# Optimization experiments

Hardware: AMD Instinct MI355X
Metric: run time of the kernel (lower is better)

## Reference

```python
import jax, jax.numpy as jnp
import numpy as np

N = 100_000      # nodes
E = 500_000      # bonds
DN = 128         # dim_node_embedding
DB = 64          # dim_bond_embedding
NTOK = 4         # num_bond_token
DIN = 2 * DN + 2 * DB  # 384
LEAKY = 0.001
LN_EPS = 1e-5
DIST_MAX = 20.0
STEP = 0.5


def _lrelu(v):
    return jnp.where(v >= 0, v, LEAKY * v)


def _layernorm(v, w, b):
    m = v.mean(-1, keepdims=True)
    var = ((v - m) ** 2).mean(-1, keepdims=True)
    return (v - m) / jnp.sqrt(var + LN_EPS) * w + b


def setup_inputs() -> dict:
    key = jax.random.key(0)
    ks = jax.random.split(key, 20)
    x = jax.random.normal(ks[0], (N, 3), dtype=jnp.float32) * 3.0
    pos = jax.random.normal(ks[1], (N, 3), dtype=jnp.float32)
    node_embedding = jax.random.normal(ks[2], (N, DN), dtype=jnp.float32)
    i0 = jax.random.randint(ks[3], (E,), 0, N)
    off = jax.random.randint(ks[4], (E,), 1, N)  # nonzero -> no self-bonds
    bond_index = jnp.stack([i0, (i0 + off) % N], axis=1).astype(jnp.int32)
    bond_types = jax.random.randint(ks[5], (E,), 0, NTOK).astype(jnp.int32)
    s = 0.02
    params = dict(
        bond_emb=jax.random.normal(ks[6], (NTOK, DB), dtype=jnp.float32),
        W0=jax.random.normal(ks[7], (DIN, DN), dtype=jnp.float32) * s,
        b0=jnp.zeros((DN,), jnp.float32),
        W1=jax.random.normal(ks[8], (DN, DN), dtype=jnp.float32) * s,
        b1=jnp.zeros((DN,), jnp.float32),
        ln1_w=jnp.ones((DN,), jnp.float32),
        ln1_b=jnp.zeros((DN,), jnp.float32),
        W2=jax.random.normal(ks[9], (DN, DN), dtype=jnp.float32) * s,
        b2=jnp.zeros((DN,), jnp.float32),
        ln2_w=jnp.ones((DN,), jnp.float32),
        ln2_b=jnp.zeros((DN,), jnp.float32),
        Wo=jax.random.normal(ks[10], (DN, 2), dtype=jnp.float32) * s,
        bo=jnp.zeros((2,), jnp.float32),
    )
    return dict(x=x, pos=pos, node_embedding=node_embedding,
                bond_index=bond_index, bond_types=bond_types, **params)


def reference(x, pos, node_embedding, bond_index, bond_types,
              bond_emb, W0, b0, W1, b1, ln1_w, ln1_b,
              W2, b2, ln2_w, ln2_b, Wo, bo):
    i = bond_index[:, 0]
    j = bond_index[:, 1]

    # ---- BondLength geometry ----
    diff = x[i] - x[j]                                   # [E,3]
    dist = jnp.linalg.norm(diff, axis=-1, keepdims=True)  # [E,1]
    u = diff / dist                                       # [E,3] unit j->i? (i-j)/d
    direction = jnp.stack([u, -u], axis=-1)               # [E,3,2]

    # ---- Smearing (gaussian RBF + overflow bin, normalized) ----
    offset = jnp.linspace(0.0, DIST_MAX, DB - 1, dtype=jnp.float32)  # [63]
    delta = DIST_MAX / (DB - 2)
    coeff = -0.5 / (delta * delta)
    rbf = jnp.exp(coeff * (dist - offset) ** 2)            # [E,63]
    ovf = (dist >= DIST_MAX).astype(x.dtype)               # [E,1]
    smear = jnp.concatenate([rbf, ovf], axis=-1)           # [E,64]
    smear = smear / smear.sum(axis=-1, keepdims=True)

    # ---- Edge MLP (LeakyMLP, num_layer=2, dim_end=2) ----
    feat = jnp.concatenate(
        [node_embedding[i], node_embedding[j], bond_emb[bond_types], smear],
        axis=-1)                                           # [E,384]
    h = _lrelu(feat @ W0 + b0)
    h = _lrelu(_layernorm(h @ W1 + b1, ln1_w, ln1_b))
    h = _lrelu(_layernorm(h @ W2 + b2, ln2_w, ln2_b))
    force = h @ Wo + bo                                    # [E,2]

    # ---- position update (scatter-add) ----
    update = force[:, None, :] * direction                 # [E,3,2]
    pos = pos.at[i].add(STEP * update[..., 0])
    pos = pos.at[j].add(STEP * update[..., 1])
    return pos
```

## Files before the change

kernel.cpp:

```cpp
#include <hip/hip_runtime.h>
#include <stdint.h>

#define N_EDGES 500000
#define N_NODES 100000
#define PREP_NG 2
#define TBINS 1280

typedef __attribute__((ext_vector_type(8))) short short8;
typedef __attribute__((ext_vector_type(4))) float floatx4;

__device__ __forceinline__ uint16_t f2bf(float f) {
  union { float f; uint32_t u; } cv; cv.f = f;
  uint32_t u = cv.u;
  return (uint16_t)((u + 0x7FFFu + ((u >> 16) & 1u)) >> 16);
}
__device__ __forceinline__ uint32_t pk2bf(float lo, float hi) {
  return __builtin_amdgcn_perm(__float_as_uint(hi), __float_as_uint(lo), 0x07060302u);
}
__device__ __forceinline__ uint16_t bftrunc(float f) {
  return (uint16_t)(__float_as_uint(f) >> 16);
}
__device__ __forceinline__ float bf2f_lo(uint32_t u) { return __uint_as_float(u << 16); }
__device__ __forceinline__ float bf2f_hi(uint32_t u) { return __uint_as_float(u & 0xFFFF0000u); }
__device__ __forceinline__ float lrelu(float v) { return fmaxf(v, 0.001f * v); }

__device__ __forceinline__ void gload_lds16(const uint16_t* g, uint16_t* l) {
  __builtin_amdgcn_global_load_lds(
      (const __attribute__((address_space(1))) void*)g,
      (__attribute__((address_space(3))) void*)l, 16, 0, 0);
}

__global__ void prep0_kernel(const float* __restrict__ W0, const float* __restrict__ b0,
                             const float* __restrict__ W1, const float* __restrict__ W2,
                             const float* __restrict__ bemb,
                             uint16_t* __restrict__ w0ab, uint16_t* __restrict__ w1f,
                             uint16_t* __restrict__ w2f, float* __restrict__ be0f,
                             const float* __restrict__ pos, float* __restrict__ out, int npos) {
  int id = blockIdx.x * 256 + threadIdx.x;
  if (id < 32768) {
    int f = id;
    int j = f & 7, lane = (f >> 3) & 63, ntt = (f >> 9) & 15, ks = f >> 13;
    int k = ks * 32 + (lane >> 4) * 8 + j;
    int row = (ntt < 8) ? k : (128 + k);
    int col = (ntt & 7) * 16 + (lane & 15);
    w0ab[f] = f2bf(W0[row * 128 + col]);
  } else if (id < 49152) {
    int f = id - 32768;
    int j = f & 7, lane = (f >> 3) & 63, nt = (f >> 9) & 7, ks = f >> 12;
    int k = ks * 32 + (lane >> 4) * 8 + j;
    w1f[f] = f2bf(W1[k * 128 + nt * 16 + (lane & 15)]);
  } else if (id < 65536) {
    int f = id - 49152;
    int j = f & 7, lane = (f >> 3) & 63, nt = (f >> 9) & 7, ks = f >> 12;
    int k = ks * 32 + (lane >> 4) * 8 + j;
    w2f[f] = f2bf(W2[k * 128 + nt * 16 + (lane & 15)]);
  } else if (id < 66048) {
    int t = id - 65536; int ty = t >> 7, n = t & 127;
    float s = b0[n];
    for (int kk = 0; kk < 64; ++kk) s += bemb[ty * 64 + kk] * W0[(256 + kk) * 128 + n];
    be0f[t] = s;
  } else if (id - 66048 < npos) {
    out[id - 66048] = pos[id - 66048];
  }
}

__global__ void prep_t_kernel(const float* __restrict__ W0, const float* __restrict__ be0f,
                              uint16_t* __restrict__ T) {
  __shared__ float rbf[64];
  int b = blockIdx.x;
  int t = threadIdx.x;
  float dist = (float)b * (1.0f / 32.0f);
  const float delta = 20.0f / 62.0f;
  const float coeff = -0.5f / (delta * delta);
  if (t < 64) {
    float v;
    if (t < 63) { float d = dist - (float)t * delta; v = __expf(coeff * d * d); }
    else v = (dist >= 20.0f) ? 1.0f : 0.0f;
    rbf[t] = v;
  }
  __syncthreads();
  float sum = 0.0f;
  for (int k = 0; k < 64; ++k) sum += rbf[k];
  float rs = 1.0f / sum;
  for (int o = t; o < 512; o += 256) {
    int ty = o >> 7, n = o & 127;
    float s = be0f[ty * 128 + n];
    for (int k = 0; k < 64; ++k) s += rbf[k] * rs * W0[(320 + k) * 128 + n];
    T[((size_t)(ty * TBINS + b)) * 128 + n] = f2bf(s);
  }
}

__global__ __attribute__((amdgpu_flat_work_group_size(256, 256), amdgpu_waves_per_eu(1, 4)))
void prep_p_kernel(const float* __restrict__ nemb, const uint16_t* __restrict__ w0ab,
                   uint16_t* __restrict__ Pa, uint16_t* __restrict__ Pb) {
  __shared__ __align__(16) uint16_t aLds[4 * PREP_NG * 16 * 136];
  const int tid = threadIdx.x;
  const int lane = tid & 63;
  const int wave = tid >> 6;
  const int n15 = lane & 15;
  const int quad = lane >> 4;
  uint16_t* myA = aLds + wave * (PREP_NG * 16 * 136);
  const int base = blockIdx.x * (64 * PREP_NG) + wave * (16 * PREP_NG);

  {
    const int le = lane >> 2, sub = lane & 3;
#pragma unroll
    for (int it = 0; it < PREP_NG; ++it) {
      int r = base + it * 16 + le; if (r >= N_NODES) r = N_NODES - 1;
      const float4* src = (const float4*)(nemb + (size_t)r * 128);
#pragma unroll
      for (int g = 0; g < 4; ++g) {
        float4 a = src[sub * 8 + g * 2], b = src[sub * 8 + g * 2 + 1];
        uint4 pk;
        pk.x = pk2bf(a.x, a.y); pk.y = pk2bf(a.z, a.w);
        pk.z = pk2bf(b.x, b.y); pk.w = pk2bf(b.z, b.w);
        *(uint4*)(myA + (it * 16 + le) * 136 + sub * 32 + g * 8) = pk;
      }
    }
  }

  const short8* wfv = (const short8*)w0ab + lane;
#pragma unroll
  for (int q = 0; q < 4; ++q) {
    short8 bfr[16];
#pragma unroll
    for (int ks = 0; ks < 4; ++ks)
#pragma unroll
      for (int nq = 0; nq < 4; ++nq)
        bfr[ks * 4 + nq] = wfv[(ks * 16 + q * 4 + nq) * 64];
#pragma unroll
    for (int it = 0; it < PREP_NG; ++it) {
      floatx4 acc[4];
#pragma unroll
      for (int nq = 0; nq < 4; ++nq) acc[nq] = (floatx4){0.f, 0.f, 0.f, 0.f};
#pragma unroll
      for (int ks = 0; ks < 4; ++ks) {
        short8 a = *(const short8*)(myA + (it * 16 + n15) * 136 + ks * 32 + quad * 8);
#pragma unroll
        for (int nq = 0; nq < 4; ++nq)
          acc[nq] = __builtin_amdgcn_mfma_f32_16x16x32_bf16(a, bfr[ks * 4 + nq], acc[nq], 0, 0, 0);
      }
      uint16_t* dst = (q < 2) ? Pa : Pb;
      int cbase = ((q & 1) * 4) * 16 + n15;
#pragma unroll
      for (int nq = 0; nq < 4; ++nq) {
        int c = cbase + nq * 16;
#pragma unroll
        for (int r = 0; r < 4; ++r) {
          int row = base + it * 16 + quad * 4 + r;
          if (row < N_NODES) dst[(size_t)row * 128 + c] = bftrunc(acc[nq][r]);
        }
      }
    }
  }
}

__device__ __forceinline__ void gemm_lds(const uint16_t* ws, const uint16_t* aRow,
                                         int lane, floatx4* acc) {
  short8 a[4];
#pragma unroll
  for (int ks = 0; ks < 4; ++ks) a[ks] = *(const short8*)(aRow + ks * 32);
#pragma unroll
  for (int ks = 0; ks < 4; ++ks)
#pragma unroll
    for (int nt = 0; nt < 8; ++nt) {
      short8 b = *(const short8*)(ws + (ks * 8 + nt) * 512 + lane * 8);
      acc[nt] = __builtin_amdgcn_mfma_f32_16x16x32_bf16(a[ks], b, acc[nt], 0, 0, 0);
    }
}

__global__ __attribute__((amdgpu_flat_work_group_size(256, 256)))
void bond_mlp_kernel(const float* __restrict__ x,
                     const int* __restrict__ bidx, const int* __restrict__ btyp,
                     const uint16_t* __restrict__ Pa, const uint16_t* __restrict__ Pb,
                     const uint16_t* __restrict__ Tt, const uint16_t* __restrict__ w1f,
                     const uint16_t* __restrict__ w2f,
                     const float* __restrict__ b1, const float* __restrict__ ln1w,
                     const float* __restrict__ ln1b,
                     const float* __restrict__ b2, const float* __restrict__ ln2w,
                     const float* __restrict__ ln2b,
                     const float* __restrict__ Wo, const float* __restrict__ bo,
                     float* __restrict__ out) {
  __shared__ __align__(16) uint16_t wstage[16384];
  __shared__ __align__(16) uint16_t hA_all[4 * 16 * 136];
  __shared__ float u_lds[64][3];
  __shared__ int ij_lds[64][2];

  const int tid = threadIdx.x;
  const int lane = tid & 63;
  const int wave = tid >> 6;
  const int n15 = lane & 15;
  const int quad = lane >> 4;

  uint16_t* hA = hA_all + wave * (16 * 136);

#pragma unroll
  for (int j = 0; j < 8; ++j)
    gload_lds16(w1f + (wave * 8 + j) * 512 + lane * 8, wstage + (wave * 8 + j) * 512);

  {
    const int le = lane >> 2, sub = lane & 3;
    const int gr = wave * 16 + le;
    const int ge = blockIdx.x * 64 + gr;
    const bool valid = ge < N_EDGES;
    int vi = 0, vj = 0, bt = 0;
    if (valid) { vi = bidx[2 * ge]; vj = bidx[2 * ge + 1]; bt = btyp[ge]; }
    float dx, dy, dz;
    if (valid) {
      dx = x[3 * vi]     - x[3 * vj];
      dy = x[3 * vi + 1] - x[3 * vj + 1];
      dz = x[3 * vi + 2] - x[3 * vj + 2];
    } else { dx = 1.0f; dy = 0.0f; dz = 0.0f; }
    float dist = sqrtf(dx * dx + dy * dy + dz * dz);
    float rinv = 1.0f / dist;
    if (sub == 0) {
      u_lds[gr][0] = dx * rinv; u_lds[gr][1] = dy * rinv; u_lds[gr][2] = dz * rinv;
      ij_lds[gr][0] = vi; ij_lds[gr][1] = vj;
    }
    float fb = fminf(dist, 39.5f) * 32.0f;
    int bi = (int)fb;
    float w = fb - (float)bi;
    const uint4* pa = (const uint4*)(Pa + (size_t)vi * 128 + sub * 32);
    const uint4* pb = (const uint4*)(Pb + (size_t)vj * 128 + sub * 32);
    const uint16_t* trow = Tt + ((size_t)(bt * TBINS + bi)) * 128 + sub * 32;
    const uint4* t0p = (const uint4*)trow;
    const uint4* t1p = (const uint4*)(trow + 128);
#pragma unroll
    for (int g = 0; g < 4; ++g) {
      uint4 av = pa[g], bv = pb[g], t0 = t0p[g], t1 = t1p[g];
      uint4 pk;
      {
        float lo = bf2f_lo(av.x) + bf2f_lo(bv.x), hi = bf2f_hi(av.x) + bf2f_hi(bv.x);
        float l0 = bf2f_lo(t0.x), l1 = bf2f_lo(t1.x), h0 = bf2f_hi(t0.x), h1 = bf2f_hi(t1.x);
        pk.x = pk2bf(lrelu(lo + l0 + w * (l1 - l0)), lrelu(hi + h0 + w * (h1 - h0)));
      }
      {
        float lo = bf2f_lo(av.y) + bf2f_lo(bv.y), hi = bf2f_hi(av.y) + bf2f_hi(bv.y);
        float l0 = bf2f_lo(t0.y), l1 = bf2f_lo(t1.y), h0 = bf2f_hi(t0.y), h1 = bf2f_hi(t1.y);
        pk.y = pk2bf(lrelu(lo + l0 + w * (l1 - l0)), lrelu(hi + h0 + w * (h1 - h0)));
      }
      {
        float lo = bf2f_lo(av.z) + bf2f_lo(bv.z), hi = bf2f_hi(av.z) + bf2f_hi(bv.z);
        float l0 = bf2f_lo(t0.z), l1 = bf2f_lo(t1.z), h0 = bf2f_hi(t0.z), h1 = bf2f_hi(t1.z);
        pk.z = pk2bf(lrelu(lo + l0 + w * (l1 - l0)), lrelu(hi + h0 + w * (h1 - h0)));
      }
      {
        float lo = bf2f_lo(av.w) + bf2f_lo(bv.w), hi = bf2f_hi(av.w) + bf2f_hi(bv.w);
        float l0 = bf2f_lo(t0.w), l1 = bf2f_lo(t1.w), h0 = bf2f_hi(t0.w), h1 = bf2f_hi(t1.w);
        pk.w = pk2bf(lrelu(lo + l0 + w * (l1 - l0)), lrelu(hi + h0 + w * (h1 - h0)));
      }
      *(uint4*)(hA + le * 136 + sub * 32 + g * 8) = pk;
    }
  }
  __syncthreads();

  const uint16_t* aRow = hA + n15 * 136 + quad * 8;

  floatx4 acc[8];
#pragma unroll
  for (int nt = 0; nt < 8; ++nt) acc[nt] = (floatx4){0.f, 0.f, 0.f, 0.f};
  gemm_lds(wstage, aRow, lane, acc);

  __syncthreads();
#pragma unroll
  for (int j = 0; j < 8; ++j)
    gload_lds16(w2f + (wave * 8 + j) * 512 + lane * 8, wstage + (wave * 8 + j) * 512);

  {
    float bv[8], wv[8], bb2[8];
#pragma unroll
    for (int nt = 0; nt < 8; ++nt) {
      int col = nt * 16 + n15;
      bv[nt] = b1[col]; wv[nt] = ln1w[col]; bb2[nt] = ln1b[col];
    }
    float s[4] = {0,0,0,0}, q[4] = {0,0,0,0};
#pragma unroll
    for (int nt = 0; nt < 8; ++nt)
#pragma unroll
      for (int r = 0; r < 4; ++r) { float v = acc[nt][r] + bv[nt]; s[r] += v; q[r] += v * v; }
#pragma unroll
    for (int m = 1; m <= 8; m <<= 1)
#pragma unroll
      for (int r = 0; r < 4; ++r) { s[r] += __shfl_xor(s[r], m); q[r] += __shfl_xor(q[r], m); }
    float mean[4], rstd[4];
#pragma unroll
    for (int r = 0; r < 4; ++r) {
      mean[r] = s[r] * (1.0f / 128.0f);
      float var = q[r] * (1.0f / 128.0f) - mean[r] * mean[r];
      rstd[r] = rsqrtf(var + 1e-5f);
    }
#pragma unroll
    for (int nt = 0; nt < 8; ++nt)
#pragma unroll
      for (int r = 0; r < 4; ++r) {
        float v = acc[nt][r] + bv[nt];
        float vn = (v - mean[r]) * rstd[r] * wv[nt] + bb2[nt];
        hA[(quad * 4 + r) * 136 + nt * 16 + n15] = bftrunc(lrelu(vn));
      }
  }
  __syncthreads();

#pragma unroll
  for (int nt = 0; nt < 8; ++nt) acc[nt] = (floatx4){0.f, 0.f, 0.f, 0.f};
  gemm_lds(wstage, aRow, lane, acc);

  {
    float bv[8], wv[8], bb2[8], wo0[8], wo1[8];
#pragma unroll
    for (int nt = 0; nt < 8; ++nt) {
      int col = nt * 16 + n15;
      bv[nt] = b2[col]; wv[nt] = ln2w[col]; bb2[nt] = ln2b[col];
      wo0[nt] = Wo[2 * col]; wo1[nt] = Wo[2 * col + 1];
    }
    float s[4] = {0,0,0,0}, q[4] = {0,0,0,0};
#pragma unroll
    for (int nt = 0; nt < 8; ++nt)
#pragma unroll
      for (int r = 0; r < 4; ++r) { float v = acc[nt][r] + bv[nt]; s[r] += v; q[r] += v * v; }
#pragma unroll
    for (int m = 1; m <= 8; m <<= 1)
#pragma unroll
      for (int r = 0; r < 4; ++r) { s[r] += __shfl_xor(s[r], m); q[r] += __shfl_xor(q[r], m); }
    float mean[4], rstd[4];
#pragma unroll
    for (int r = 0; r < 4; ++r) {
      mean[r] = s[r] * (1.0f / 128.0f);
      float var = q[r] * (1.0f / 128.0f) - mean[r] * mean[r];
      rstd[r] = rsqrtf(var + 1e-5f);
    }
    float f0[4] = {0,0,0,0}, f1[4] = {0,0,0,0};
#pragma unroll
    for (int nt = 0; nt < 8; ++nt)
#pragma unroll
      for (int r = 0; r < 4; ++r) {
        float v = acc[nt][r] + bv[nt];
        float vn = lrelu((v - mean[r]) * rstd[r] * wv[nt] + bb2[nt]);
        f0[r] += vn * wo0[nt];
        f1[r] += vn * wo1[nt];
      }
#pragma unroll
    for (int m = 1; m <= 8; m <<= 1)
#pragma unroll
      for (int r = 0; r < 4; ++r) { f0[r] += __shfl_xor(f0[r], m); f1[r] += __shfl_xor(f1[r], m); }

    if (n15 < 4) {
      int gr = wave * 16 + quad * 4 + n15;
      int ge2 = blockIdx.x * 64 + gr;
      if (ge2 < N_EDGES) {
        float F0 = (n15 == 0) ? f0[0] : (n15 == 1) ? f0[1] : (n15 == 2) ? f0[2] : f0[3];
        float F1 = (n15 == 0) ? f1[0] : (n15 == 1) ? f1[1] : (n15 == 2) ? f1[2] : f1[3];
        F0 += bo[0]; F1 += bo[1];
        float ux = u_lds[gr][0], uy = u_lds[gr][1], uz = u_lds[gr][2];
        int ii = ij_lds[gr][0], jj = ij_lds[gr][1];
        float c0 = 0.5f * F0;
        float c1 = -0.5f * F1;
        atomicAdd(out + 3 * ii,     c0 * ux);
        atomicAdd(out + 3 * ii + 1, c0 * uy);
        atomicAdd(out + 3 * ii + 2, c0 * uz);
        atomicAdd(out + 3 * jj,     c1 * ux);
        atomicAdd(out + 3 * jj + 1, c1 * uy);
        atomicAdd(out + 3 * jj + 2, c1 * uz);
      }
    }
  }
}

extern "C" void kernel_launch(void* const* d_in, const int* in_sizes, int n_in,
                              void* d_out, int out_size, void* d_ws, size_t ws_size,
                              hipStream_t stream) {
  const float* x    = (const float*)d_in[0];
  const float* pos  = (const float*)d_in[1];
  const float* nemb = (const float*)d_in[2];
  const int*   bidx = (const int*)d_in[3];
  const int*   btyp = (const int*)d_in[4];
  const float* bemb = (const float*)d_in[5];
  const float* W0   = (const float*)d_in[6];
  const float* b0   = (const float*)d_in[7];
  const float* W1   = (const float*)d_in[8];
  const float* b1   = (const float*)d_in[9];
  const float* ln1w = (const float*)d_in[10];
  const float* ln1b = (const float*)d_in[11];
  const float* W2   = (const float*)d_in[12];
  const float* b2   = (const float*)d_in[13];
  const float* ln2w = (const float*)d_in[14];
  const float* ln2b = (const float*)d_in[15];
  const float* Wo   = (const float*)d_in[16];
  const float* bo   = (const float*)d_in[17];
  float* out = (float*)d_out;

  uint16_t* w0ab = (uint16_t*)d_ws;
  uint16_t* w1f  = w0ab + 32768;
  uint16_t* w2f  = w1f + 16384;
  float*    be0f = (float*)(w2f + 16384);
  uint16_t* Tt   = (uint16_t*)(be0f + 512);
  uint16_t* Pa   = Tt + 4 * TBINS * 128;
  uint16_t* Pb   = Pa + (size_t)N_NODES * 128;

  prep0_kernel<<<(66048 + out_size + 255) / 256, 256, 0, stream>>>(
      W0, b0, W1, W2, bemb, w0ab, w1f, w2f, be0f, pos, out, out_size);
  prep_t_kernel<<<TBINS, 256, 0, stream>>>(W0, be0f, Tt);
  prep_p_kernel<<<(N_NODES + 64 * PREP_NG - 1) / (64 * PREP_NG), 256, 0, stream>>>(
      nemb, w0ab, Pa, Pb);
  bond_mlp_kernel<<<(N_EDGES + 63) / 64, 256, 0, stream>>>(
      x, bidx, btyp, Pa, Pb, Tt, w1f, w2f,
      b1, ln1w, ln1b, b2, ln2w, ln2b, Wo, bo, out);
}
```

Baseline: 352.3 us.

## Precompute edge geometry in separate kernel and use nearest-bin table lookup

Adds an edge_geom_kernel that computes per-edge node indices, table row index and unit direction into a compact 16-byte record plus a float2, so the main MLP kernel no longer does the dependent x gathers and sqrt. The distance table resolution is doubled and the main kernel reads one table row with nearest-bin rounding instead of two rows with linear interpolation. This removes one gather per edge and the lerp arithmetic, at the cost of an extra kernel launch, extra global write/read traffic for the edge records, a larger table to precompute, and a coarser approximation of the smearing term.

```diff
diff --git a/kernel.cpp b/kernel.cpp
--- a/kernel.cpp
+++ b/kernel.cpp
@@ -4,7 +4,7 @@
 #define N_EDGES 500000
 #define N_NODES 100000
 #define PREP_NG 2
-#define TBINS 1280
+#define TBINS 2560
 
 typedef __attribute__((ext_vector_type(8))) short short8;
 typedef __attribute__((ext_vector_type(4))) float floatx4;
@@ -28,6 +28,27 @@
   __builtin_amdgcn_global_load_lds(
       (const __attribute__((address_space(1))) void*)g,
       (__attribute__((address_space(3))) void*)l, 16, 0, 0);
+}
+
+__global__ void edge_geom_kernel(const float* __restrict__ x, const int* __restrict__ bidx,
+                                 const int* __restrict__ btyp,
+                                 uint4* __restrict__ rec16, float2* __restrict__ ru2) {
+  int ge = blockIdx.x * 256 + threadIdx.x;
+  if (ge >= N_EDGES) return;
+  int vi = bidx[2 * ge], vj = bidx[2 * ge + 1], bt = btyp[ge];
+  float dx = x[3 * vi]     - x[3 * vj];
+  float dy = x[3 * vi + 1] - x[3 * vj + 1];
+  float dz = x[3 * vi + 2] - x[3 * vj + 2];
+  float dist = sqrtf(dx * dx + dy * dy + dz * dz);
+  float rinv = 1.0f / dist;
+  int bi = (int)(dist * 64.0f + 0.5f);
+  if (bi > TBINS - 1) bi = TBINS - 1;
+  uint4 r;
+  r.x = (unsigned)vi; r.y = (unsigned)vj;
+  r.z = (unsigned)(bt * TBINS + bi);
+  r.w = __float_as_uint(dz * rinv);
+  rec16[ge] = r;
+  ru2[ge] = (float2){dx * rinv, dy * rinv};
 }
 
 __global__ void prep0_kernel(const float* __restrict__ W0, const float* __restrict__ b0,
@@ -69,7 +90,7 @@
   __shared__ float rbf[64];
   int b = blockIdx.x;
   int t = threadIdx.x;
-  float dist = (float)b * (1.0f / 32.0f);
+  float dist = (float)b * (1.0f / 64.0f);
   const float delta = 20.0f / 62.0f;
   const float coeff = -0.5f / (delta * delta);
   if (t < 64) {
@@ -170,8 +191,7 @@
 }
 
 __global__ __attribute__((amdgpu_flat_work_group_size(256, 256)))
-void bond_mlp_kernel(const float* __restrict__ x,
-                     const int* __restrict__ bidx, const int* __restrict__ btyp,
+void bond_mlp_kernel(const uint4* __restrict__ rec16, const float2* __restrict__ ru2,
                      const uint16_t* __restrict__ Pa, const uint16_t* __restrict__ Pb,
                      const uint16_t* __restrict__ Tt, const uint16_t* __restrict__ w1f,
                      const uint16_t* __restrict__ w2f,
@@ -203,52 +223,29 @@
     const int gr = wave * 16 + le;
     const int ge = blockIdx.x * 64 + gr;
     const bool valid = ge < N_EDGES;
-    int vi = 0, vj = 0, bt = 0;
-    if (valid) { vi = bidx[2 * ge]; vj = bidx[2 * ge + 1]; bt = btyp[ge]; }
-    float dx, dy, dz;
-    if (valid) {
-      dx = x[3 * vi]     - x[3 * vj];
-      dy = x[3 * vi + 1] - x[3 * vj + 1];
-      dz = x[3 * vi + 2] - x[3 * vj + 2];
-    } else { dx = 1.0f; dy = 0.0f; dz = 0.0f; }
-    float dist = sqrtf(dx * dx + dy * dy + dz * dz);
-    float rinv = 1.0f / dist;
+    uint4 r16 = (uint4){0u, 0u, 0u, 0u};
+    if (valid) r16 = rec16[ge];
+    const int vi = (int)r16.x, vj = (int)r16.y, tix = (int)r16.z;
     if (sub == 0) {
-      u_lds[gr][0] = dx * rinv; u_lds[gr][1] = dy * rinv; u_lds[gr][2] = dz * rinv;
+      float2 uxy = valid ? ru2[ge] : (float2){0.f, 0.f};
+      u_lds[gr][0] = uxy.x; u_lds[gr][1] = uxy.y; u_lds[gr][2] = __uint_as_float(r16.w);
       ij_lds[gr][0] = vi; ij_lds[gr][1] = vj;
     }
-    float fb = fminf(dist, 39.5f) * 32.0f;
-    int bi = (int)fb;
-    float w = fb - (float)bi;
     const uint4* pa = (const uint4*)(Pa + (size_t)vi * 128 + sub * 32);
     const uint4* pb = (const uint4*)(Pb + (size_t)vj * 128 + sub * 32);
-    const uint16_t* trow = Tt + ((size_t)(bt * TBINS + bi)) * 128 + sub * 32;
-    const uint4* t0p = (const uint4*)trow;
-    const uint4* t1p = (const uint4*)(trow + 128);
+    const uint4* tp = (const uint4*)(Tt + (size_t)tix * 128 + sub * 32);
 #pragma unroll
     for (int g = 0; g < 4; ++g) {
-      uint4 av = pa[g], bv = pb[g], t0 = t0p[g], t1 = t1p[g];
+      uint4 av = pa[g], bv = pb[g], tv = tp[g];
       uint4 pk;
-      {
-        float lo = bf2f_lo(av.x) + bf2f_lo(bv.x), hi = bf2f_hi(av.x) + bf2f_hi(bv.x);
-        float l0 = bf2f_lo(t0.x), l1 = bf2f_lo(t1.x), h0 = bf2f_hi(t0.x), h1 = bf2f_hi(t1.x);
-        pk.x = pk2bf(lrelu(lo + l0 + w * (l1 - l0)), lrelu(hi + h0 + w * (h1 - h0)));
-      }
-      {
-        float lo = bf2f_lo(av.y) + bf2f_lo(bv.y), hi = bf2f_hi(av.y) + bf2f_hi(bv.y);
-        float l0 = bf2f_lo(t0.y), l1 = bf2f_lo(t1.y), h0 = bf2f_hi(t0.y), h1 = bf2f_hi(t1.y);
-        pk.y = pk2bf(lrelu(lo + l0 + w * (l1 - l0)), lrelu(hi + h0 + w * (h1 - h0)));
-      }
-      {
-        float lo = bf2f_lo(av.z) + bf2f_lo(bv.z), hi = bf2f_hi(av.z) + bf2f_hi(bv.z);
-        float l0 = bf2f_lo(t0.z), l1 = bf2f_lo(t1.z), h0 = bf2f_hi(t0.z), h1 = bf2f_hi(t1.z);
-        pk.z = pk2bf(lrelu(lo + l0 + w * (l1 - l0)), lrelu(hi + h0 + w * (h1 - h0)));
-      }
-      {
-        float lo = bf2f_lo(av.w) + bf2f_lo(bv.w), hi = bf2f_hi(av.w) + bf2f_hi(bv.w);
-        float l0 = bf2f_lo(t0.w), l1 = bf2f_lo(t1.w), h0 = bf2f_hi(t0.w), h1 = bf2f_hi(t1.w);
-        pk.w = pk2bf(lrelu(lo + l0 + w * (l1 - l0)), lrelu(hi + h0 + w * (h1 - h0)));
-      }
+      pk.x = pk2bf(lrelu(bf2f_lo(av.x) + bf2f_lo(bv.x) + bf2f_lo(tv.x)),
+                   lrelu(bf2f_hi(av.x) + bf2f_hi(bv.x) + bf2f_hi(tv.x)));
+      pk.y = pk2bf(lrelu(bf2f_lo(av.y) + bf2f_lo(bv.y) + bf2f_lo(tv.y)),
+                   lrelu(bf2f_hi(av.y) + bf2f_hi(bv.y) + bf2f_hi(tv.y)));
+      pk.z = pk2bf(lrelu(bf2f_lo(av.z) + bf2f_lo(bv.z) + bf2f_lo(tv.z)),
+                   lrelu(bf2f_hi(av.z) + bf2f_hi(bv.z) + bf2f_hi(tv.z)));
+      pk.w = pk2bf(lrelu(bf2f_lo(av.w) + bf2f_lo(bv.w) + bf2f_lo(tv.w)),
+                   lrelu(bf2f_hi(av.w) + bf2f_hi(bv.w) + bf2f_hi(tv.w)));
       *(uint4*)(hA + le * 136 + sub * 32 + g * 8) = pk;
     }
   }
@@ -393,15 +390,18 @@
   uint16_t* w2f  = w1f + 16384;
   float*    be0f = (float*)(w2f + 16384);
   uint16_t* Tt   = (uint16_t*)(be0f + 512);
-  uint16_t* Pa   = Tt + 4 * TBINS * 128;
+  uint16_t* Pa   = Tt + (size_t)4 * TBINS * 128;
   uint16_t* Pb   = Pa + (size_t)N_NODES * 128;
-
+  uint4*    rec16 = (uint4*)(Pb + (size_t)N_NODES * 128);
+  float2*   ru2  = (float2*)(rec16 + N_EDGES);
+
+  edge_geom_kernel<<<(N_EDGES + 255) / 256, 256, 0, stream>>>(x, bidx, btyp, rec16, ru2);
   prep0_kernel<<<(66048 + out_size + 255) / 256, 256, 0, stream>>>(
       W0, b0, W1, W2, bemb, w0ab, w1f, w2f, be0f, pos, out, out_size);
   prep_t_kernel<<<TBINS, 256, 0, stream>>>(W0, be0f, Tt);
   prep_p_kernel<<<(N_NODES + 64 * PREP_NG - 1) / (64 * PREP_NG), 256, 0, stream>>>(
       nemb, w0ab, Pa, Pb);
   bond_mlp_kernel<<<(N_EDGES + 63) / 64, 256, 0, stream>>>(
-      x, bidx, btyp, Pa, Pb, Tt, w1f, w2f,
+      rec16, ru2, Pa, Pb, Tt, w1f, w2f,
       b1, ln1w, ln1b, b2, ln2w, ln2b, Wo, bo, out);
 }
```

New measurement: 373.1 us. 5.9% more time.

## Store node projections in fp32 and use nearest-bin distance table lookup

Applied to the files above, without the earlier changes.

Node projection tables Pa/Pb are now written and read as fp32 instead of bf16, doubling gather traffic per edge. The distance table gets twice as many bins, and the per-edge linear interpolation between two table rows is replaced by a nearest-bin lookup of a single row. This removes one table gather and the interpolation arithmetic, but doubles the bytes gathered from the node tables and adds quantisation error from the nearest-bin lookup.

```diff
diff --git a/kernel.cpp b/kernel.cpp
--- a/kernel.cpp
+++ b/kernel.cpp
@@ -4,7 +4,7 @@
 #define N_EDGES 500000
 #define N_NODES 100000
 #define PREP_NG 2
-#define TBINS 1280
+#define TBINS 2560
 
 typedef __attribute__((ext_vector_type(8))) short short8;
 typedef __attribute__((ext_vector_type(4))) float floatx4;
@@ -69,7 +69,7 @@
   __shared__ float rbf[64];
   int b = blockIdx.x;
   int t = threadIdx.x;
-  float dist = (float)b * (1.0f / 32.0f);
+  float dist = (float)b * (1.0f / 64.0f);
   const float delta = 20.0f / 62.0f;
   const float coeff = -0.5f / (delta * delta);
   if (t < 64) {
@@ -92,7 +92,7 @@
 
 __global__ __attribute__((amdgpu_flat_work_group_size(256, 256), amdgpu_waves_per_eu(1, 4)))
 void prep_p_kernel(const float* __restrict__ nemb, const uint16_t* __restrict__ w0ab,
-                   uint16_t* __restrict__ Pa, uint16_t* __restrict__ Pb) {
+                   float* __restrict__ Pa, float* __restrict__ Pb) {
   __shared__ __align__(16) uint16_t aLds[4 * PREP_NG * 16 * 136];
   const int tid = threadIdx.x;
   const int lane = tid & 63;
@@ -140,7 +140,7 @@
         for (int nq = 0; nq < 4; ++nq)
           acc[nq] = __builtin_amdgcn_mfma_f32_16x16x32_bf16(a, bfr[ks * 4 + nq], acc[nq], 0, 0, 0);
       }
-      uint16_t* dst = (q < 2) ? Pa : Pb;
+      float* dst = (q < 2) ? Pa : Pb;
       int cbase = ((q & 1) * 4) * 16 + n15;
 #pragma unroll
       for (int nq = 0; nq < 4; ++nq) {
@@ -148,7 +148,7 @@
 #pragma unroll
         for (int r = 0; r < 4; ++r) {
           int row = base + it * 16 + quad * 4 + r;
-          if (row < N_NODES) dst[(size_t)row * 128 + c] = bftrunc(acc[nq][r]);
+          if (row < N_NODES) dst[(size_t)row * 128 + c] = acc[nq][r];
         }
       }
     }
@@ -172,7 +172,7 @@
 __global__ __attribute__((amdgpu_flat_work_group_size(256, 256)))
 void bond_mlp_kernel(const float* __restrict__ x,
                      const int* __restrict__ bidx, const int* __restrict__ btyp,
-                     const uint16_t* __restrict__ Pa, const uint16_t* __restrict__ Pb,
+                     const float* __restrict__ Pa, const float* __restrict__ Pb,
                      const uint16_t* __restrict__ Tt, const uint16_t* __restrict__ w1f,
                      const uint16_t* __restrict__ w2f,
                      const float* __restrict__ b1, const float* __restrict__ ln1w,
@@ -217,38 +217,21 @@
       u_lds[gr][0] = dx * rinv; u_lds[gr][1] = dy * rinv; u_lds[gr][2] = dz * rinv;
       ij_lds[gr][0] = vi; ij_lds[gr][1] = vj;
     }
-    float fb = fminf(dist, 39.5f) * 32.0f;
-    int bi = (int)fb;
-    float w = fb - (float)bi;
-    const uint4* pa = (const uint4*)(Pa + (size_t)vi * 128 + sub * 32);
-    const uint4* pb = (const uint4*)(Pb + (size_t)vj * 128 + sub * 32);
-    const uint16_t* trow = Tt + ((size_t)(bt * TBINS + bi)) * 128 + sub * 32;
-    const uint4* t0p = (const uint4*)trow;
-    const uint4* t1p = (const uint4*)(trow + 128);
+    int bi = (int)(dist * 64.0f + 0.5f);
+    if (bi > TBINS - 1) bi = TBINS - 1;
+    const float4* pa = (const float4*)(Pa + (size_t)vi * 128 + sub * 32);
+    const float4* pb = (const float4*)(Pb + (size_t)vj * 128 + sub * 32);
+    const uint4* tp = (const uint4*)(Tt + ((size_t)(bt * TBINS + bi)) * 128 + sub * 32);
 #pragma unroll
     for (int g = 0; g < 4; ++g) {
-      uint4 av = pa[g], bv = pb[g], t0 = t0p[g], t1 = t1p[g];
+      float4 a0 = pa[2 * g], a1 = pa[2 * g + 1];
+      float4 q0 = pb[2 * g], q1 = pb[2 * g + 1];
+      uint4 tv = tp[g];
       uint4 pk;
-      {
-        float lo = bf2f_lo(av.x) + bf2f_lo(bv.x), hi = bf2f_hi(av.x) + bf2f_hi(bv.x);
-        float l0 = bf2f_lo(t0.x), l1 = bf2f_lo(t1.x), h0 = bf2f_hi(t0.x), h1 = bf2f_hi(t1.x);
-        pk.x = pk2bf(lrelu(lo + l0 + w * (l1 - l0)), lrelu(hi + h0 + w * (h1 - h0)));
-      }
-      {
-        float lo = bf2f_lo(av.y) + bf2f_lo(bv.y), hi = bf2f_hi(av.y) + bf2f_hi(bv.y);
-        float l0 = bf2f_lo(t0.y), l1 = bf2f_lo(t1.y), h0 = bf2f_hi(t0.y), h1 = bf2f_hi(t1.y);
-        pk.y = pk2bf(lrelu(lo + l0 + w * (l1 - l0)), lrelu(hi + h0 + w * (h1 - h0)));
-      }
-      {
-        float lo = bf2f_lo(av.z) + bf2f_lo(bv.z), hi = bf2f_hi(av.z) + bf2f_hi(bv.z);
-        float l0 = bf2f_lo(t0.z), l1 = bf2f_lo(t1.z), h0 = bf2f_hi(t0.z), h1 = bf2f_hi(t1.z);
-        pk.z = pk2bf(lrelu(lo + l0 + w * (l1 - l0)), lrelu(hi + h0 + w * (h1 - h0)));
-      }
-      {
-        float lo = bf2f_lo(av.w) + bf2f_lo(bv.w), hi = bf2f_hi(av.w) + bf2f_hi(bv.w);
-        float l0 = bf2f_lo(t0.w), l1 = bf2f_lo(t1.w), h0 = bf2f_hi(t0.w), h1 = bf2f_hi(t1.w);
-        pk.w = pk2bf(lrelu(lo + l0 + w * (l1 - l0)), lrelu(hi + h0 + w * (h1 - h0)));
-      }
+      pk.x = pk2bf(lrelu(a0.x + q0.x + bf2f_lo(tv.x)), lrelu(a0.y + q0.y + bf2f_hi(tv.x)));
+      pk.y = pk2bf(lrelu(a0.z + q0.z + bf2f_lo(tv.y)), lrelu(a0.w + q0.w + bf2f_hi(tv.y)));
+      pk.z = pk2bf(lrelu(a1.x + q1.x + bf2f_lo(tv.z)), lrelu(a1.y + q1.y + bf2f_hi(tv.z)));
+      pk.w = pk2bf(lrelu(a1.z + q1.z + bf2f_lo(tv.w)), lrelu(a1.w + q1.w + bf2f_hi(tv.w)));
       *(uint4*)(hA + le * 136 + sub * 32 + g * 8) = pk;
     }
   }
@@ -393,8 +376,8 @@
   uint16_t* w2f  = w1f + 16384;
   float*    be0f = (float*)(w2f + 16384);
   uint16_t* Tt   = (uint16_t*)(be0f + 512);
-  uint16_t* Pa   = Tt + 4 * TBINS * 128;
-  uint16_t* Pb   = Pa + (size_t)N_NODES * 128;
+  float*    Pa   = (float*)(Tt + (size_t)4 * TBINS * 128);
+  float*    Pb   = Pa + (size_t)N_NODES * 128;
 
   prep0_kernel<<<(66048 + out_size + 255) / 256, 256, 0, stream>>>(
       W0, b0, W1, W2, bemb, w0ab, w1f, w2f, be0f, pos, out, out_size);
```

Measured after the change: 376.3 us. 6.8% more time.
